# Optimization experiments

Hardware: AMD Instinct MI355X
Metric: run time of the kernel (lower is better)

## Reference

```python
import jax, jax.numpy as jnp
import numpy as np
import math


def _mirror_even(x):
    # even-symmetric extension: [..., H, W] -> [..., 2H, 2W]
    x = jnp.concatenate([x, jnp.flip(x, -1)], axis=-1)
    return jnp.concatenate([x, jnp.flip(x, -2)], axis=-2)


def _grad_img(x):
    # Fourier-domain spectral gradient on the even-symmetric extension,
    # matching PoissonCompositionLayer.grad_img (wx = arange(1,2W+1)-(W+1) = arange(-W,W)).
    H, W = x.shape[-2], x.shape[-1]
    kx = jnp.arange(-W, W)[None, :]          # [1, 2W]
    ky = jnp.arange(-H, H)[:, None]          # [2H, 1]
    dft = jnp.fft.fftshift(jnp.fft.fft2(_mirror_even(x)), axes=(-1, -2))
    gx = jnp.fft.ifft2(jnp.fft.fftshift((2j * math.pi / (2 * W)) * kx * dft, axes=(-1, -2))).real
    gy = jnp.fft.ifft2(jnp.fft.fftshift((2j * math.pi / (2 * H)) * ky * dft, axes=(-1, -2))).real
    return gx[..., :H, :W], gy[..., :H, :W]


def setup_inputs() -> dict:
    key = jax.random.key(0)
    k1, k2, k3 = jax.random.split(key, 3)
    B, C, H, W = 2, 3, 512, 512
    target = jax.random.normal(k1, (B, C, H, W), dtype=jnp.float32)
    source = jax.random.normal(k2, (B, C, H, W), dtype=jnp.float32)
    mask = jax.random.uniform(k3, (B, C, H, W), dtype=jnp.float32)
    return {"target": target, "source": source, "mask": mask}


def reference(target, source, mask):
    H, W = target.shape[-2], target.shape[-1]
    # composite gradient field
    gxt, gyt = _grad_img(target)
    gxs, gys = _grad_img(source)
    gx = (1.0 - mask) * gxt + mask * gxs
    gy = (1.0 - mask) * gyt + mask * gys
    # odd extension in x / even in y for gx; odd in y / even in x for gy
    gxp = jnp.concatenate([gx, -jnp.flip(gx, -1)], axis=-1)
    gxp = jnp.concatenate([gxp, jnp.flip(gxp, -2)], axis=-2)
    gyp = jnp.concatenate([gy, -jnp.flip(gy, -2)], axis=-2)
    gyp = jnp.concatenate([gyp, jnp.flip(gyp, -1)], axis=-1)
    dx = jnp.fft.fftshift(jnp.fft.fft2(gxp), axes=(-1, -2))
    dy = jnp.fft.fftshift(jnp.fft.fft2(gyp), axes=(-1, -2))
    # shifted frequency grids (DC sits at index [H, W])
    kx = jnp.arange(-W, W)[None, :]
    ky = jnp.arange(-H, H)[:, None]
    fx = 2j * math.pi * kx / (2 * W)
    fy = 2j * math.pi * ky / (2 * H)
    coeff = (fx * dx + fy * dy) / (fx ** 2 + fy ** 2 + 1e-10)
    coeff = coeff.at[..., H, W].set(0.0)  # zero DC component
    u = jnp.fft.ifft2(jnp.fft.fftshift(coeff, axes=(-1, -2)))
    res = u.real[..., :H, :W]
    # mean-matching on the unmasked region; original uses batch index 0's means for all batches
    inv = 1.0 - mask
    denom = jnp.sum(inv, axis=(-1, -2))                       # [B, C]
    mean1 = jnp.sum(target * inv, axis=(-1, -2)) / denom      # [B, C]
    mean2 = jnp.sum(res * inv, axis=(-1, -2)) / denom         # [B, C]
    return res + (mean1[0] - mean2[0])[None, :, None, None]
```

## Files before the change

kernel.cpp:

```cpp
#include <hip/hip_runtime.h>


#define CH 262144
#define NCH 6
#define NTOT (NCH*CH)

typedef _Float16 f16x8 __attribute__((ext_vector_type(8)));
typedef float f32x4  __attribute__((ext_vector_type(4)));

static constexpr float kPi        = 3.14159265358979323846f;
static constexpr float kPiOver512 = 0.006135923151542565f;
static constexpr float kPi2Norm   = 3.7649933338155804e-05f;
static constexpr float kInvHW     = 3.814697265625e-06f;

__device__ __forceinline__ void hst(float v, short* p) {
    *reinterpret_cast<_Float16*>(p) = (_Float16)v;
}

__device__ __forceinline__ float hfun(int k) {
    if (k == 0) return 0.f;
    float sgn = 1.f;
    if (k < 0) { k = -k; sgn = -1.f; }
    if (k > 512) { k = 1024 - k; sgn = -sgn; }
    float sv, cv;
    sincosf((float)k * (kPi / 1024.0f), &sv, &cv);
    float v = cv / sv;
    if (k & 1) v = -v;
    return sgn * v;
}

__global__ void build_tables(short* Mc, short* Ms, short* McT, short* GT) {
    int idx = blockIdx.x * blockDim.x + threadIdx.x;
    if (idx >= CH) return;
    int a = idx >> 9, b = idx & 511;
    int p1 = (a * (2 * b + 1)) & 2047;
    float s1, c1; sincosf((float)p1 * (kPi / 1024.0f), &s1, &c1);
    hst(c1, Mc + idx);
    hst(s1, Ms + idx);
    int p2 = (b * (2 * a + 1)) & 2047;
    float s2, c2; sincosf((float)p2 * (kPi / 1024.0f), &s2, &c2);
    hst(c2, McT + idx);
    float g = (kPi / 1024.0f) * (hfun(a + b + 1) + hfun(a - b));
    hst(g, GT + idx);
}

__device__ __forceinline__ void gl_lds16(const short* g, const short* l) {
    __builtin_amdgcn_global_load_lds(
        (const __attribute__((address_space(1))) void*)g,
        (__attribute__((address_space(3))) void*)l, 16, 0, 0);
}

#define FOFF(r, j) (((r) << 6) + 8 * ((j) ^ ((r) & 7)))

#define MFMA16(a, b, c) __builtin_amdgcn_mfma_f32_16x16x32_f16(a, b, c, 0, 0, 0)

template<int OM>
__global__ __launch_bounds__(256) void gemm_tn(
    const short* __restrict__ A0, int sA0, const short* __restrict__ B0, int sB0,
    float* __restrict__ Cf0, short* __restrict__ O0, int sC0,
    const short* __restrict__ A1, int sA1, const short* __restrict__ B1, int sB1,
    float* __restrict__ Cf1, short* __restrict__ O1, int sC1,
    int zsplit, const float* __restrict__ msk, float* __restrict__ redp)
{
    __shared__ short LS[2][2][4096];
    int z = blockIdx.z;
    const short *A, *B; float* Cf; short* O;
    if (z < zsplit) {
        A = A0 + (size_t)z * sA0; B = B0 + (size_t)z * sB0;
        Cf = Cf0 ? Cf0 + (size_t)z * sC0 : nullptr;
        O  = O0 ? O0 + (size_t)z * sC0 : nullptr;
    } else {
        int zz = z - zsplit;
        A = A1 + (size_t)zz * sA1; B = B1 + (size_t)zz * sB1;
        Cf = Cf1 ? Cf1 + (size_t)zz * sC1 : nullptr;
        O  = O1 ? O1 + (size_t)zz * sC1 : nullptr;
    }
    int tid = threadIdx.x;
    int l = tid & 63, w = tid >> 6;
    int m0 = blockIdx.y * 64, n0 = blockIdx.x * 64;

    int srow = w * 8 + (l >> 3);
    int skc  = (l & 7) ^ ((l >> 3) & 7);
    const short* gA = A + (size_t)(m0 + srow) * 512 + 8 * skc;
    const short* gB = B + (size_t)(n0 + srow) * 512 + 8 * skc;

    int wr = w >> 1, wc = w & 1;
    int lr = l & 15, lc = l >> 4;
    int rA0 = wr * 32 + lr, rA1 = rA0 + 16;
    int rB0 = wc * 32 + lr, rB1 = rB0 + 16;

    f32x4 a00 = {0,0,0,0}, a01 = a00, a10 = a00, a11 = a00;

#define STAGE_AB(nb, k0) \
    gl_lds16(gA + (k0), &LS[nb][0][w * 512]); \
    gl_lds16(gA + (k0) + 32 * 512, &LS[nb][0][w * 512 + 2048]); \
    gl_lds16(gB + (k0), &LS[nb][1][w * 512]); \
    gl_lds16(gB + (k0) + 32 * 512, &LS[nb][1][w * 512 + 2048]);

    STAGE_AB(0, 0)
    __syncthreads();

    for (int step = 0; step < 8; ++step) {
        int buf = step & 1;
        if (step < 7) { STAGE_AB(buf ^ 1, (step + 1) * 64) }
#pragma unroll
        for (int ks = 0; ks < 2; ++ks) {
            int j = lc + 4 * ks;
            f16x8 va0 = *(const f16x8*)&LS[buf][0][FOFF(rA0, j)];
            f16x8 va1 = *(const f16x8*)&LS[buf][0][FOFF(rA1, j)];
            f16x8 vb0 = *(const f16x8*)&LS[buf][1][FOFF(rB0, j)];
            f16x8 vb1 = *(const f16x8*)&LS[buf][1][FOFF(rB1, j)];
            a00 = MFMA16(va0, vb0, a00);
            a01 = MFMA16(va0, vb1, a01);
            a10 = MFMA16(va1, vb0, a10);
            a11 = MFMA16(va1, vb1, a11);
        }
        __syncthreads();
    }
#undef STAGE_AB

    int crow = m0 + wr * 32 + lc * 4;
    int ccol = n0 + wc * 32 + lr;
    const f32x4* accs[2][2] = {{&a00, &a01}, {&a10, &a11}};
    float lsum = 0.f;
#pragma unroll
    for (int q = 0; q < 2; ++q)
#pragma unroll
        for (int pp = 0; pp < 2; ++pp)
#pragma unroll
            for (int rr = 0; rr < 4; ++rr) {
                int idx = (crow + q * 16 + rr) * 512 + ccol + pp * 16;
                float v = (*accs[q][pp])[rr];
                if (OM == 1) {
                    hst(v, O + idx);
                } else {
                    Cf[idx] = v;
                    lsum += v * (1.0f - msk[(size_t)z * CH + idx]);
                }
            }
    if (OM == 2) {
        float* red = (float*)LS;
        red[tid] = lsum;
        __syncthreads();
        for (int s2 = 128; s2 > 0; s2 >>= 1) {
            if (tid < s2) red[tid] += red[tid + s2];
            __syncthreads();
        }
        if (tid == 0) redp[z * 64 + blockIdx.y * 8 + blockIdx.x] = red[0];
    }
}

__global__ __launch_bounds__(256) void gemm_l1(
    const short* __restrict__ dn, const short* __restrict__ dt,
    const short* __restrict__ GT, const float* __restrict__ msk,
    short* __restrict__ C_, short* __restrict__ D_)
{
    __shared__ short LS[2][2][4096];
    int z = blockIdx.z;
    bool gxp = z < 6;
    int zz = gxp ? z : z - 6;
    const short* A = (gxp ? dn : dt) + (size_t)zz * CH;
    const float* mz = msk + (size_t)zz * CH;

    int tid = threadIdx.x;
    int l = tid & 63, w = tid >> 6;
    int m0 = blockIdx.y * 64, n0 = blockIdx.x * 64;

    int srow = w * 8 + (l >> 3);
    int skc  = (l & 7) ^ ((l >> 3) & 7);
    const short* gA = A + (size_t)(m0 + srow) * 512 + 8 * skc;
    const short* gB = GT + (size_t)(n0 + srow) * 512 + 8 * skc;

    int wr = w >> 1, wc = w & 1;
    int lr = l & 15, lc = l >> 4;
    int rA0 = wr * 32 + lr, rA1 = rA0 + 16;
    int rB0 = wc * 32 + lr, rB1 = rB0 + 16;

    f32x4 a00 = {0,0,0,0}, a01 = a00, a10 = a00, a11 = a00;

#define STAGE_AB(nb, k0) \
    gl_lds16(gA + (k0), &LS[nb][0][w * 512]); \
    gl_lds16(gA + (k0) + 32 * 512, &LS[nb][0][w * 512 + 2048]); \
    gl_lds16(gB + (k0), &LS[nb][1][w * 512]); \
    gl_lds16(gB + (k0) + 32 * 512, &LS[nb][1][w * 512 + 2048]);

    STAGE_AB(0, 0)
    __syncthreads();

    for (int step = 0; step < 8; ++step) {
        int buf = step & 1;
        if (step < 7) { STAGE_AB(buf ^ 1, (step + 1) * 64) }
#pragma unroll
        for (int ks = 0; ks < 2; ++ks) {
            int j = lc + 4 * ks;
            f16x8 va0 = *(const f16x8*)&LS[buf][0][FOFF(rA0, j)];
            f16x8 va1 = *(const f16x8*)&LS[buf][0][FOFF(rA1, j)];
            f16x8 vb0 = *(const f16x8*)&LS[buf][1][FOFF(rB0, j)];
            f16x8 vb1 = *(const f16x8*)&LS[buf][1][FOFF(rB1, j)];
            a00 = MFMA16(va0, vb0, a00);
            a01 = MFMA16(va0, vb1, a01);
            a10 = MFMA16(va1, vb0, a10);
            a11 = MFMA16(va1, vb1, a11);
        }
        __syncthreads();
    }
#undef STAGE_AB

    const f32x4* accs[2][2] = {{&a00, &a01}, {&a10, &a11}};
    float* tile = (float*)LS;

    if (gxp) {
        short* o = C_ + (size_t)zz * CH;
#pragma unroll
        for (int q = 0; q < 2; ++q)
#pragma unroll
            for (int pp = 0; pp < 2; ++pp)
#pragma unroll
                for (int rr = 0; rr < 4; ++rr) {
                    int r = wr * 32 + lc * 4 + q * 16 + rr;
                    int c = wc * 32 + pp * 16 + lr;
                    float v = (*accs[q][pp])[rr] * mz[(size_t)(m0 + r) * 512 + n0 + c];
                    tile[c * 65 + r] = v;
                }
        __syncthreads();
#pragma unroll
        for (int pass = 0; pass < 16; ++pass) {
            int jj = pass * 4 + (tid >> 6);
            int ii = tid & 63;
            hst(tile[jj * 65 + ii], o + (n0 + jj) * 512 + m0 + ii);
        }
    } else {
        short* o = D_ + (size_t)zz * CH;
#pragma unroll
        for (int pass = 0; pass < 16; ++pass) {
            int ii = pass * 4 + (tid >> 6);
            int jj = tid & 63;
            tile[jj * 65 + ii] = mz[(size_t)(n0 + ii) * 512 + m0 + jj];
        }
        __syncthreads();
#pragma unroll
        for (int q = 0; q < 2; ++q)
#pragma unroll
            for (int pp = 0; pp < 2; ++pp)
#pragma unroll
                for (int rr = 0; rr < 4; ++rr) {
                    int r = wr * 32 + lc * 4 + q * 16 + rr;
                    int c = wc * 32 + pp * 16 + lr;
                    float v = (*accs[q][pp])[rr] * tile[r * 65 + c];
                    hst(v, o + (m0 + r) * 512 + n0 + c);
                }
    }
}

__global__ __launch_bounds__(256) void gemm_l3(
    const short* __restrict__ Ms, const short* __restrict__ Mc,
    const short* __restrict__ P, const short* __restrict__ Q,
    short* __restrict__ O_)
{
    __shared__ short LS[2][4][4096];
    int z = blockIdx.z;
    const short* pz = P + (size_t)z * CH;
    const short* qz = Q + (size_t)z * CH;
    short* o = O_ + (size_t)z * CH;

    int tid = threadIdx.x;
    int l = tid & 63, w = tid >> 6;
    int m0 = blockIdx.y * 64, n0 = blockIdx.x * 64;

    int srow = w * 8 + (l >> 3);
    int skc  = (l & 7) ^ ((l >> 3) & 7);
    size_t ga = (size_t)(m0 + srow) * 512 + 8 * skc;
    size_t gb = (size_t)(n0 + srow) * 512 + 8 * skc;
    const short* g0 = Ms + ga;
    const short* g1 = Mc + ga;
    const short* g2 = pz + gb;
    const short* g3 = qz + gb;

    int wr = w >> 1, wc = w & 1;
    int lr = l & 15, lc = l >> 4;
    int rA0 = wr * 32 + lr, rA1 = rA0 + 16;
    int rB0 = wc * 32 + lr, rB1 = rB0 + 16;

    f32x4 x00 = {0,0,0,0}, x01 = x00, x10 = x00, x11 = x00;
    f32x4 y00 = x00, y01 = x00, y10 = x00, y11 = x00;

#define STAGE_L3(nb, k0) \
    gl_lds16(g0 + (k0), &LS[nb][0][w * 512]); \
    gl_lds16(g0 + (k0) + 32 * 512, &LS[nb][0][w * 512 + 2048]); \
    gl_lds16(g1 + (k0), &LS[nb][1][w * 512]); \
    gl_lds16(g1 + (k0) + 32 * 512, &LS[nb][1][w * 512 + 2048]); \
    gl_lds16(g2 + (k0), &LS[nb][2][w * 512]); \
    gl_lds16(g2 + (k0) + 32 * 512, &LS[nb][2][w * 512 + 2048]); \
    gl_lds16(g3 + (k0), &LS[nb][3][w * 512]); \
    gl_lds16(g3 + (k0) + 32 * 512, &LS[nb][3][w * 512 + 2048]);

    STAGE_L3(0, 0)
    __syncthreads();

    for (int step = 0; step < 8; ++step) {
        int buf = step & 1;
        if (step < 7) { STAGE_L3(buf ^ 1, (step + 1) * 64) }
#pragma unroll
        for (int ks = 0; ks < 2; ++ks) {
            int j = lc + 4 * ks;
            f16x8 s0 = *(const f16x8*)&LS[buf][0][FOFF(rA0, j)];
            f16x8 s1 = *(const f16x8*)&LS[buf][0][FOFF(rA1, j)];
            f16x8 p0 = *(const f16x8*)&LS[buf][2][FOFF(rB0, j)];
            f16x8 p1 = *(const f16x8*)&LS[buf][2][FOFF(rB1, j)];
            x00 = MFMA16(s0, p0, x00);
            x01 = MFMA16(s0, p1, x01);
            x10 = MFMA16(s1, p0, x10);
            x11 = MFMA16(s1, p1, x11);
            f16x8 c0 = *(const f16x8*)&LS[buf][1][FOFF(rA0, j)];
            f16x8 c1 = *(const f16x8*)&LS[buf][1][FOFF(rA1, j)];
            f16x8 q0 = *(const f16x8*)&LS[buf][3][FOFF(rB0, j)];
            f16x8 q1 = *(const f16x8*)&LS[buf][3][FOFF(rB1, j)];
            y00 = MFMA16(c0, q0, y00);
            y01 = MFMA16(c0, q1, y01);
            y10 = MFMA16(c1, q0, y10);
            y11 = MFMA16(c1, q1, y11);
        }
        __syncthreads();
    }
#undef STAGE_L3

    int crow = m0 + wr * 32 + lc * 4;
    int ccol = n0 + wc * 32 + lr;
    const f32x4* xs[2][2] = {{&x00, &x01}, {&x10, &x11}};
    const f32x4* ys[2][2] = {{&y00, &y01}, {&y10, &y11}};
#pragma unroll
    for (int q = 0; q < 2; ++q)
#pragma unroll
        for (int pp = 0; pp < 2; ++pp) {
            int u = ccol + pp * 16;
            float eu = (u ? 2.0f : 1.0f) * kInvHW;
#pragma unroll
            for (int rr = 0; rr < 4; ++rr) {
                int v = crow + q * 16 + rr;
                float gx = (*xs[q][pp])[rr];
                float gy = (*ys[q][pp])[rr];
                float num = kPiOver512 * ((float)v * gx + (float)u * gy);
                float den = 1e-10f - kPi2Norm * (float)(u * u + v * v);
                float eps = (v ? 2.0f : 1.0f) * eu;
                hst(eps * num / den, o + v * 512 + u);
            }
        }
}

__global__ __launch_bounds__(256) void diff_split_red(
    const float* __restrict__ s, const float* __restrict__ t, const float* __restrict__ m,
    short* __restrict__ dn, short* __restrict__ dt,
    float* __restrict__ mt, float* __restrict__ mi)
{
    __shared__ float tile[32][33];
    __shared__ float red[512];
    int z = blockIdx.z;
    const float* sz = s + (size_t)z * CH;
    const float* tz = t + (size_t)z * CH;
    const float* mz = m + (size_t)z * CH;
    short* nh = dn + (size_t)z * CH;
    short* th = dt + (size_t)z * CH;
    int bx = blockIdx.x * 32, by = blockIdx.y * 32;
    int tx = threadIdx.x & 31, ty = threadIdx.x >> 5;
    float accT = 0.f, accI = 0.f;
    for (int r = ty; r < 32; r += 8) {
        int idx = (by + r) * 512 + bx + tx;
        float tv = tz[idx];
        float d = sz[idx] - tv;
        tile[r][tx] = d;
        hst(d, nh + idx);
        accT += tv;
        if (z < 3) accI += 1.0f - mz[idx];
    }
    __syncthreads();
    for (int r = ty; r < 32; r += 8) {
        hst(tile[tx][r], th + (bx + r) * 512 + by + tx);
    }
    int tid = threadIdx.x;
    red[tid] = accT; red[256 + tid] = accI;
    __syncthreads();
    for (int s2 = 128; s2 > 0; s2 >>= 1) {
        if (tid < s2) { red[tid] += red[tid + s2]; red[256 + tid] += red[256 + tid + s2]; }
        __syncthreads();
    }
    if (tid == 0) {
        int tileid = blockIdx.y * 16 + blockIdx.x;
        mt[z * 256 + tileid] = red[0];
        if (z < 3) mi[z * 256 + tileid] = red[256];
    }
}

__global__ __launch_bounds__(256) void final_out(
    const float* __restrict__ t, const float* __restrict__ U,
    const float* __restrict__ part, float* __restrict__ out)
{
    __shared__ float mtv[6], wmuv[3];
    int tid = threadIdx.x;
    if (tid < 6) {
        float s2 = 0.f;
        for (int k = 0; k < 256; ++k) s2 += part[tid * 256 + k];
        mtv[tid] = s2 * (1.0f / (float)CH);
    }
    if (tid >= 8 && tid < 11) {
        int c = tid - 8;
        float si = 0.f, su = 0.f;
        for (int k = 0; k < 256; ++k) si += part[1536 + c * 256 + k];
        for (int k = 0; k < 64; ++k) su += part[2304 + c * 64 + k];
        wmuv[c] = su / si;
    }
    __syncthreads();
    int n4 = NTOT / 4;
    for (int i = blockIdx.x * blockDim.x + tid; i < n4; i += gridDim.x * blockDim.x) {
        int z = i >> 16;
        int c = z % 3;
        float sh = -mtv[z] + mtv[c] - wmuv[c];
        float4 tv = ((const float4*)t)[i];
        float4 uv = ((const float4*)U)[i];
        ((float4*)out)[i] = make_float4(tv.x + uv.x + sh, tv.y + uv.y + sh,
                                        tv.z + uv.z + sh, tv.w + uv.w + sh);
    }
}

extern "C" void kernel_launch(void* const* d_in, const int* in_sizes, int n_in,
                              void* d_out, int out_size, void* d_ws, size_t ws_size,
                              hipStream_t stream) {
    const float* t = (const float*)d_in[0];
    const float* s = (const float*)d_in[1];
    const float* m = (const float*)d_in[2];
    float* out = (float*)d_out;
    float* F = (float*)d_ws;
    if (ws_size < (size_t)(21 * CH + 4096) * sizeof(float)) return;

    short* T = (short*)F;
    short *Mc = T, *Ms = T + (size_t)CH, *McT = T + 2 * (size_t)CH, *GT = T + 3 * (size_t)CH;
    short* A_ = (short*)(F + 2  * (size_t)CH);
    short* B_ = (short*)(F + 5  * (size_t)CH);
    short* C_ = (short*)(F + 8  * (size_t)CH);
    short* D_ = (short*)(F + 11 * (size_t)CH);
    float* F0  = F + 14 * (size_t)CH;
    float* part = F + 20 * (size_t)CH;

    build_tables<<<1024, 256, 0, stream>>>(Mc, Ms, McT, GT);

    diff_split_red<<<dim3(16, 16, 6), 256, 0, stream>>>(s, t, m, A_, B_,
                                                        part, part + 1536);

    gemm_l1<<<dim3(8, 8, 12), 256, 0, stream>>>(A_, B_, GT, m, C_, D_);

    gemm_tn<1><<<dim3(8, 8, 12), 256, 0, stream>>>(
        Mc, 0, C_, CH, nullptr, A_, CH,
        Ms, 0, D_, CH, nullptr, B_, CH, 6, nullptr, nullptr);

    gemm_l3<<<dim3(8, 8, 6), 256, 0, stream>>>(Ms, Mc, A_, B_, C_);

    gemm_tn<1><<<dim3(8, 8, 6), 256, 0, stream>>>(
        McT, 0, C_, CH, nullptr, D_, CH,
        McT, 0, C_, CH, nullptr, D_, CH, 6, nullptr, nullptr);

    gemm_tn<2><<<dim3(8, 8, 6), 256, 0, stream>>>(
        D_, CH, McT, 0, F0, nullptr, CH,
        D_, CH, McT, 0, F0, nullptr, CH, 6, m, part + 2304);

    final_out<<<768, 256, 0, stream>>>(t, F0, part, out);
}
```

Measured before the change: 70.39 us.

## Pre-swizzle constant DCT tables into MFMA fragment order and fuse table build

The constant cosine/sine/gradient tables are now generated directly in MFMA operand-fragment order, so every GEMM kernel reads them straight from global memory into registers instead of staging them through LDS. This halves the LDS staging traffic and LDS footprint per block. The separate table-building launch is merged into the difference/reduction kernel as an extra z-slice, removing one kernel launch. The cost is that the per-k-step direct global loads of table fragments now sit in the MFMA loop and may expose latency that LDS prefetch previously hid.

Measured after the change: 77.95 us. 10.7% more time.

```diff
diff --git a/kernel.cpp b/kernel.cpp
--- a/kernel.cpp
+++ b/kernel.cpp
@@ -29,21 +29,6 @@
     return sgn * v;
 }
 
-__global__ void build_tables(short* Mc, short* Ms, short* McT, short* GT) {
-    int idx = blockIdx.x * blockDim.x + threadIdx.x;
-    if (idx >= CH) return;
-    int a = idx >> 9, b = idx & 511;
-    int p1 = (a * (2 * b + 1)) & 2047;
-    float s1, c1; sincosf((float)p1 * (kPi / 1024.0f), &s1, &c1);
-    hst(c1, Mc + idx);
-    hst(s1, Ms + idx);
-    int p2 = (b * (2 * a + 1)) & 2047;
-    float s2, c2; sincosf((float)p2 * (kPi / 1024.0f), &s2, &c2);
-    hst(c2, McT + idx);
-    float g = (kPi / 1024.0f) * (hfun(a + b + 1) + hfun(a - b));
-    hst(g, GT + idx);
-}
-
 __device__ __forceinline__ void gl_lds16(const short* g, const short* l) {
     __builtin_amdgcn_global_load_lds(
         (const __attribute__((address_space(1))) void*)g,
@@ -51,27 +36,26 @@
 }
 
 #define FOFF(r, j) (((r) << 6) + 8 * ((j) ^ ((r) & 7)))
-
 #define MFMA16(a, b, c) __builtin_amdgcn_mfma_f32_16x16x32_f16(a, b, c, 0, 0, 0)
 
-template<int OM>
+template<int OM, int TA>
 __global__ __launch_bounds__(256) void gemm_tn(
-    const short* __restrict__ A0, int sA0, const short* __restrict__ B0, int sB0,
+    const short* __restrict__ T0, const short* __restrict__ X0, int sX0,
     float* __restrict__ Cf0, short* __restrict__ O0, int sC0,
-    const short* __restrict__ A1, int sA1, const short* __restrict__ B1, int sB1,
+    const short* __restrict__ T1, const short* __restrict__ X1, int sX1,
     float* __restrict__ Cf1, short* __restrict__ O1, int sC1,
     int zsplit, const float* __restrict__ msk, float* __restrict__ redp)
 {
-    __shared__ short LS[2][2][4096];
+    __shared__ short LS[2][4352];
     int z = blockIdx.z;
-    const short *A, *B; float* Cf; short* O;
+    const short *T, *X; float* Cf; short* O;
     if (z < zsplit) {
-        A = A0 + (size_t)z * sA0; B = B0 + (size_t)z * sB0;
+        T = T0; X = X0 + (size_t)z * sX0;
         Cf = Cf0 ? Cf0 + (size_t)z * sC0 : nullptr;
         O  = O0 ? O0 + (size_t)z * sC0 : nullptr;
     } else {
         int zz = z - zsplit;
-        A = A1 + (size_t)zz * sA1; B = B1 + (size_t)zz * sB1;
+        T = T1; X = X1 + (size_t)zz * sX1;
         Cf = Cf1 ? Cf1 + (size_t)zz * sC1 : nullptr;
         O  = O1 ? O1 + (size_t)zz * sC1 : nullptr;
     }
@@ -79,45 +63,53 @@
     int l = tid & 63, w = tid >> 6;
     int m0 = blockIdx.y * 64, n0 = blockIdx.x * 64;
 
+    int xbase = TA ? n0 : m0;
     int srow = w * 8 + (l >> 3);
     int skc  = (l & 7) ^ ((l >> 3) & 7);
-    const short* gA = A + (size_t)(m0 + srow) * 512 + 8 * skc;
-    const short* gB = B + (size_t)(n0 + srow) * 512 + 8 * skc;
+    const short* gX = X + (size_t)(xbase + srow) * 512 + 8 * skc;
 
     int wr = w >> 1, wc = w & 1;
     int lr = l & 15, lc = l >> 4;
-    int rA0 = wr * 32 + lr, rA1 = rA0 + 16;
-    int rB0 = wc * 32 + lr, rB1 = rB0 + 16;
+    int rX0 = (TA ? wc : wr) * 32 + lr, rX1 = rX0 + 16;
+    int ttb = (TA ? (m0 + wr * 32) : (n0 + wc * 32)) >> 4;
+    const short* Tw0 = T + (size_t)ttb * 8192 + l * 8;
+    const short* Tw1 = Tw0 + 8192;
 
     f32x4 a00 = {0,0,0,0}, a01 = a00, a10 = a00, a11 = a00;
 
-#define STAGE_AB(nb, k0) \
-    gl_lds16(gA + (k0), &LS[nb][0][w * 512]); \
-    gl_lds16(gA + (k0) + 32 * 512, &LS[nb][0][w * 512 + 2048]); \
-    gl_lds16(gB + (k0), &LS[nb][1][w * 512]); \
-    gl_lds16(gB + (k0) + 32 * 512, &LS[nb][1][w * 512 + 2048]);
-
-    STAGE_AB(0, 0)
+#define STAGE_X(nb, k0) \
+    gl_lds16(gX + (k0), &LS[nb][w * 512]); \
+    gl_lds16(gX + (k0) + 32 * 512, &LS[nb][w * 512 + 2048]);
+
+    STAGE_X(0, 0)
     __syncthreads();
 
     for (int step = 0; step < 8; ++step) {
         int buf = step & 1;
-        if (step < 7) { STAGE_AB(buf ^ 1, (step + 1) * 64) }
+        if (step < 7) { STAGE_X(buf ^ 1, (step + 1) * 64) }
 #pragma unroll
         for (int ks = 0; ks < 2; ++ks) {
             int j = lc + 4 * ks;
-            f16x8 va0 = *(const f16x8*)&LS[buf][0][FOFF(rA0, j)];
-            f16x8 va1 = *(const f16x8*)&LS[buf][0][FOFF(rA1, j)];
-            f16x8 vb0 = *(const f16x8*)&LS[buf][1][FOFF(rB0, j)];
-            f16x8 vb1 = *(const f16x8*)&LS[buf][1][FOFF(rB1, j)];
-            a00 = MFMA16(va0, vb0, a00);
-            a01 = MFMA16(va0, vb1, a01);
-            a10 = MFMA16(va1, vb0, a10);
-            a11 = MFMA16(va1, vb1, a11);
-        }
-        __syncthreads();
-    }
-#undef STAGE_AB
+            int kc = step * 2 + ks;
+            f16x8 xf0 = *(const f16x8*)&LS[buf][FOFF(rX0, j)];
+            f16x8 xf1 = *(const f16x8*)&LS[buf][FOFF(rX1, j)];
+            f16x8 tf0 = *(const f16x8*)(Tw0 + kc * 512);
+            f16x8 tf1 = *(const f16x8*)(Tw1 + kc * 512);
+            if constexpr (TA) {
+                a00 = MFMA16(tf0, xf0, a00);
+                a01 = MFMA16(tf0, xf1, a01);
+                a10 = MFMA16(tf1, xf0, a10);
+                a11 = MFMA16(tf1, xf1, a11);
+            } else {
+                a00 = MFMA16(xf0, tf0, a00);
+                a01 = MFMA16(xf0, tf1, a01);
+                a10 = MFMA16(xf1, tf0, a10);
+                a11 = MFMA16(xf1, tf1, a11);
+            }
+        }
+        __syncthreads();
+    }
+#undef STAGE_X
 
     int crow = m0 + wr * 32 + lc * 4;
     int ccol = n0 + wc * 32 + lr;
@@ -155,11 +147,11 @@
     const short* __restrict__ GT, const float* __restrict__ msk,
     short* __restrict__ C_, short* __restrict__ D_)
 {
-    __shared__ short LS[2][2][4096];
+    __shared__ short LS[2][4352];
     int z = blockIdx.z;
     bool gxp = z < 6;
     int zz = gxp ? z : z - 6;
-    const short* A = (gxp ? dn : dt) + (size_t)zz * CH;
+    const short* X = (gxp ? dn : dt) + (size_t)zz * CH;
     const float* mz = msk + (size_t)zz * CH;
 
     int tid = threadIdx.x;
@@ -168,43 +160,43 @@
 
     int srow = w * 8 + (l >> 3);
     int skc  = (l & 7) ^ ((l >> 3) & 7);
-    const short* gA = A + (size_t)(m0 + srow) * 512 + 8 * skc;
-    const short* gB = GT + (size_t)(n0 + srow) * 512 + 8 * skc;
+    const short* gX = X + (size_t)(m0 + srow) * 512 + 8 * skc;
 
     int wr = w >> 1, wc = w & 1;
     int lr = l & 15, lc = l >> 4;
-    int rA0 = wr * 32 + lr, rA1 = rA0 + 16;
-    int rB0 = wc * 32 + lr, rB1 = rB0 + 16;
+    int rX0 = wr * 32 + lr, rX1 = rX0 + 16;
+    int ttb = (n0 + wc * 32) >> 4;
+    const short* Tw0 = GT + (size_t)ttb * 8192 + l * 8;
+    const short* Tw1 = Tw0 + 8192;
 
     f32x4 a00 = {0,0,0,0}, a01 = a00, a10 = a00, a11 = a00;
 
-#define STAGE_AB(nb, k0) \
-    gl_lds16(gA + (k0), &LS[nb][0][w * 512]); \
-    gl_lds16(gA + (k0) + 32 * 512, &LS[nb][0][w * 512 + 2048]); \
-    gl_lds16(gB + (k0), &LS[nb][1][w * 512]); \
-    gl_lds16(gB + (k0) + 32 * 512, &LS[nb][1][w * 512 + 2048]);
-
-    STAGE_AB(0, 0)
+#define STAGE_X(nb, k0) \
+    gl_lds16(gX + (k0), &LS[nb][w * 512]); \
+    gl_lds16(gX + (k0) + 32 * 512, &LS[nb][w * 512 + 2048]);
+
+    STAGE_X(0, 0)
     __syncthreads();
 
     for (int step = 0; step < 8; ++step) {
         int buf = step & 1;
-        if (step < 7) { STAGE_AB(buf ^ 1, (step + 1) * 64) }
+        if (step < 7) { STAGE_X(buf ^ 1, (step + 1) * 64) }
 #pragma unroll
         for (int ks = 0; ks < 2; ++ks) {
             int j = lc + 4 * ks;
-            f16x8 va0 = *(const f16x8*)&LS[buf][0][FOFF(rA0, j)];
-            f16x8 va1 = *(const f16x8*)&LS[buf][0][FOFF(rA1, j)];
-            f16x8 vb0 = *(const f16x8*)&LS[buf][1][FOFF(rB0, j)];
-            f16x8 vb1 = *(const f16x8*)&LS[buf][1][FOFF(rB1, j)];
-            a00 = MFMA16(va0, vb0, a00);
-            a01 = MFMA16(va0, vb1, a01);
-            a10 = MFMA16(va1, vb0, a10);
-            a11 = MFMA16(va1, vb1, a11);
-        }
-        __syncthreads();
-    }
-#undef STAGE_AB
+            int kc = step * 2 + ks;
+            f16x8 xf0 = *(const f16x8*)&LS[buf][FOFF(rX0, j)];
+            f16x8 xf1 = *(const f16x8*)&LS[buf][FOFF(rX1, j)];
+            f16x8 tf0 = *(const f16x8*)(Tw0 + kc * 512);
+            f16x8 tf1 = *(const f16x8*)(Tw1 + kc * 512);
+            a00 = MFMA16(xf0, tf0, a00);
+            a01 = MFMA16(xf0, tf1, a01);
+            a10 = MFMA16(xf1, tf0, a10);
+            a11 = MFMA16(xf1, tf1, a11);
+        }
+        __syncthreads();
+    }
+#undef STAGE_X
 
     const f32x4* accs[2][2] = {{&a00, &a01}, {&a10, &a11}};
     float* tile = (float*)LS;
@@ -257,7 +249,7 @@
     const short* __restrict__ P, const short* __restrict__ Q,
     short* __restrict__ O_)
 {
-    __shared__ short LS[2][4][4096];
+    __shared__ short LS[2][2][4096];
     int z = blockIdx.z;
     const short* pz = P + (size_t)z * CH;
     const short* qz = Q + (size_t)z * CH;
@@ -269,52 +261,49 @@
 
     int srow = w * 8 + (l >> 3);
     int skc  = (l & 7) ^ ((l >> 3) & 7);
-    size_t ga = (size_t)(m0 + srow) * 512 + 8 * skc;
-    size_t gb = (size_t)(n0 + srow) * 512 + 8 * skc;
-    const short* g0 = Ms + ga;
-    const short* g1 = Mc + ga;
-    const short* g2 = pz + gb;
-    const short* g3 = qz + gb;
+    const short* gP = pz + (size_t)(n0 + srow) * 512 + 8 * skc;
+    const short* gQ = qz + (size_t)(n0 + srow) * 512 + 8 * skc;
 
     int wr = w >> 1, wc = w & 1;
     int lr = l & 15, lc = l >> 4;
-    int rA0 = wr * 32 + lr, rA1 = rA0 + 16;
     int rB0 = wc * 32 + lr, rB1 = rB0 + 16;
+    int ttb = (m0 + wr * 32) >> 4;
+    const short* ms0p = Ms + (size_t)ttb * 8192 + l * 8;
+    const short* ms1p = ms0p + 8192;
+    const short* mc0p = Mc + (size_t)ttb * 8192 + l * 8;
+    const short* mc1p = mc0p + 8192;
 
     f32x4 x00 = {0,0,0,0}, x01 = x00, x10 = x00, x11 = x00;
     f32x4 y00 = x00, y01 = x00, y10 = x00, y11 = x00;
 
-#define STAGE_L3(nb, k0) \
-    gl_lds16(g0 + (k0), &LS[nb][0][w * 512]); \
-    gl_lds16(g0 + (k0) + 32 * 512, &LS[nb][0][w * 512 + 2048]); \
-    gl_lds16(g1 + (k0), &LS[nb][1][w * 512]); \
-    gl_lds16(g1 + (k0) + 32 * 512, &LS[nb][1][w * 512 + 2048]); \
-    gl_lds16(g2 + (k0), &LS[nb][2][w * 512]); \
-    gl_lds16(g2 + (k0) + 32 * 512, &LS[nb][2][w * 512 + 2048]); \
-    gl_lds16(g3 + (k0), &LS[nb][3][w * 512]); \
-    gl_lds16(g3 + (k0) + 32 * 512, &LS[nb][3][w * 512 + 2048]);
-
-    STAGE_L3(0, 0)
+#define STAGE_PQ(nb, k0) \
+    gl_lds16(gP + (k0), &LS[nb][0][w * 512]); \
+    gl_lds16(gP + (k0) + 32 * 512, &LS[nb][0][w * 512 + 2048]); \
+    gl_lds16(gQ + (k0), &LS[nb][1][w * 512]); \
+    gl_lds16(gQ + (k0) + 32 * 512, &LS[nb][1][w * 512 + 2048]);
+
+    STAGE_PQ(0, 0)
     __syncthreads();
 
     for (int step = 0; step < 8; ++step) {
         int buf = step & 1;
-        if (step < 7) { STAGE_L3(buf ^ 1, (step + 1) * 64) }
+        if (step < 7) { STAGE_PQ(buf ^ 1, (step + 1) * 64) }
 #pragma unroll
         for (int ks = 0; ks < 2; ++ks) {
             int j = lc + 4 * ks;
-            f16x8 s0 = *(const f16x8*)&LS[buf][0][FOFF(rA0, j)];
-            f16x8 s1 = *(const f16x8*)&LS[buf][0][FOFF(rA1, j)];
-            f16x8 p0 = *(const f16x8*)&LS[buf][2][FOFF(rB0, j)];
-            f16x8 p1 = *(const f16x8*)&LS[buf][2][FOFF(rB1, j)];
+            int kc = step * 2 + ks;
+            f16x8 p0 = *(const f16x8*)&LS[buf][0][FOFF(rB0, j)];
+            f16x8 p1 = *(const f16x8*)&LS[buf][0][FOFF(rB1, j)];
+            f16x8 s0 = *(const f16x8*)(ms0p + kc * 512);
+            f16x8 s1 = *(const f16x8*)(ms1p + kc * 512);
             x00 = MFMA16(s0, p0, x00);
             x01 = MFMA16(s0, p1, x01);
             x10 = MFMA16(s1, p0, x10);
             x11 = MFMA16(s1, p1, x11);
-            f16x8 c0 = *(const f16x8*)&LS[buf][1][FOFF(rA0, j)];
-            f16x8 c1 = *(const f16x8*)&LS[buf][1][FOFF(rA1, j)];
-            f16x8 q0 = *(const f16x8*)&LS[buf][3][FOFF(rB0, j)];
-            f16x8 q1 = *(const f16x8*)&LS[buf][3][FOFF(rB1, j)];
+            f16x8 q0 = *(const f16x8*)&LS[buf][1][FOFF(rB0, j)];
+            f16x8 q1 = *(const f16x8*)&LS[buf][1][FOFF(rB1, j)];
+            f16x8 c0 = *(const f16x8*)(mc0p + kc * 512);
+            f16x8 c1 = *(const f16x8*)(mc1p + kc * 512);
             y00 = MFMA16(c0, q0, y00);
             y01 = MFMA16(c0, q1, y01);
             y10 = MFMA16(c1, q0, y10);
@@ -322,7 +311,7 @@
         }
         __syncthreads();
     }
-#undef STAGE_L3
+#undef STAGE_PQ
 
     int crow = m0 + wr * 32 + lc * 4;
     int ccol = n0 + wc * 32 + lr;
@@ -347,14 +336,44 @@
         }
 }
 
-__global__ __launch_bounds__(256) void diff_split_red(
+__global__ __launch_bounds__(256) void diff_split_tab(
     const float* __restrict__ s, const float* __restrict__ t, const float* __restrict__ m,
     short* __restrict__ dn, short* __restrict__ dt,
+    short* __restrict__ Mc, short* __restrict__ Ms,
+    short* __restrict__ McT, short* __restrict__ GT,
     float* __restrict__ mt, float* __restrict__ mi)
 {
+    int z = blockIdx.z;
+    if (z == 6) {
+        int bid = blockIdx.y * 16 + blockIdx.x;
+        if (bid >= 128) return;
+        int g = bid * 256 + threadIdx.x;
+        int f = g >> 6, lane = g & 63;
+        int r  = ((f >> 4) << 4) | (lane & 15);
+        int kb = ((f & 15) << 5) | ((lane >> 4) << 3);
+        f16x8 vmc, vms, vmct, vgt;
+#pragma unroll
+        for (int e = 0; e < 8; ++e) {
+            int k = kb + e;
+            int p1 = (r * (2 * k + 1)) & 2047;
+            float s1, c1; sincosf((float)p1 * (kPi / 1024.0f), &s1, &c1);
+            int p2 = (k * (2 * r + 1)) & 2047;
+            float s2, c2; sincosf((float)p2 * (kPi / 1024.0f), &s2, &c2);
+            float gt = (kPi / 1024.0f) * (hfun(r + k + 1) + hfun(r - k));
+            vmc[e]  = (_Float16)c1;
+            vms[e]  = (_Float16)s1;
+            vmct[e] = (_Float16)c2;
+            vgt[e]  = (_Float16)gt;
+        }
+        *(f16x8*)(Mc  + (size_t)g * 8) = vmc;
+        *(f16x8*)(Ms  + (size_t)g * 8) = vms;
+        *(f16x8*)(McT + (size_t)g * 8) = vmct;
+        *(f16x8*)(GT  + (size_t)g * 8) = vgt;
+        return;
+    }
+
     __shared__ float tile[32][33];
     __shared__ float red[512];
-    int z = blockIdx.z;
     const float* sz = s + (size_t)z * CH;
     const float* tz = t + (size_t)z * CH;
     const float* mz = m + (size_t)z * CH;
@@ -440,26 +459,25 @@
     float* F0  = F + 14 * (size_t)CH;
     float* part = F + 20 * (size_t)CH;
 
-    build_tables<<<1024, 256, 0, stream>>>(Mc, Ms, McT, GT);
-
-    diff_split_red<<<dim3(16, 16, 6), 256, 0, stream>>>(s, t, m, A_, B_,
+    diff_split_tab<<<dim3(16, 16, 7), 256, 0, stream>>>(s, t, m, A_, B_,
+                                                        Mc, Ms, McT, GT,
                                                         part, part + 1536);
 
     gemm_l1<<<dim3(8, 8, 12), 256, 0, stream>>>(A_, B_, GT, m, C_, D_);
 
-    gemm_tn<1><<<dim3(8, 8, 12), 256, 0, stream>>>(
-        Mc, 0, C_, CH, nullptr, A_, CH,
-        Ms, 0, D_, CH, nullptr, B_, CH, 6, nullptr, nullptr);
+    gemm_tn<1, 1><<<dim3(8, 8, 12), 256, 0, stream>>>(
+        Mc, C_, CH, nullptr, A_, CH,
+        Ms, D_, CH, nullptr, B_, CH, 6, nullptr, nullptr);
 
     gemm_l3<<<dim3(8, 8, 6), 256, 0, stream>>>(Ms, Mc, A_, B_, C_);
 
-    gemm_tn<1><<<dim3(8, 8, 6), 256, 0, stream>>>(
-        McT, 0, C_, CH, nullptr, D_, CH,
-        McT, 0, C_, CH, nullptr, D_, CH, 6, nullptr, nullptr);
-
-    gemm_tn<2><<<dim3(8, 8, 6), 256, 0, stream>>>(
-        D_, CH, McT, 0, F0, nullptr, CH,
-        D_, CH, McT, 0, F0, nullptr, CH, 6, m, part + 2304);
+    gemm_tn<1, 1><<<dim3(8, 8, 6), 256, 0, stream>>>(
+        McT, C_, CH, nullptr, D_, CH,
+        McT, C_, CH, nullptr, D_, CH, 6, nullptr, nullptr);
+
+    gemm_tn<2, 0><<<dim3(8, 8, 6), 256, 0, stream>>>(
+        McT, D_, CH, F0, nullptr, CH,
+        McT, D_, CH, F0, nullptr, CH, 6, m, part + 2304);
 
     final_out<<<768, 256, 0, stream>>>(t, F0, part, out);
 }
```

## Fuse table build into split kernel and remap GEMM blocks across XCDs

Applied to the files above, without the earlier changes.

The separate build_tables launch is folded into the diff/split kernel as an extra z-slice, where each of 256 blocks computes four table entries per thread. This removes one kernel launch and lets table generation run alongside the split work. All GEMM kernels also remap their linear block id so that consecutive blocks stay on the same XCD, aiming for better L2 locality of shared operand tiles. The remap spreads work differently across chiplets and adds integer divides per block. The table slice uses fewer threads, each doing four entries serially.

Result: faster. 64.40 us (median of 2 runs) (-8.5%).

```diff
diff --git a/kernel.cpp b/kernel.cpp
--- a/kernel.cpp
+++ b/kernel.cpp
@@ -29,19 +29,14 @@
     return sgn * v;
 }
 
-__global__ void build_tables(short* Mc, short* Ms, short* McT, short* GT) {
-    int idx = blockIdx.x * blockDim.x + threadIdx.x;
-    if (idx >= CH) return;
-    int a = idx >> 9, b = idx & 511;
-    int p1 = (a * (2 * b + 1)) & 2047;
-    float s1, c1; sincosf((float)p1 * (kPi / 1024.0f), &s1, &c1);
-    hst(c1, Mc + idx);
-    hst(s1, Ms + idx);
-    int p2 = (b * (2 * a + 1)) & 2047;
-    float s2, c2; sincosf((float)p2 * (kPi / 1024.0f), &s2, &c2);
-    hst(c2, McT + idx);
-    float g = (kPi / 1024.0f) * (hfun(a + b + 1) + hfun(a - b));
-    hst(g, GT + idx);
+__device__ __forceinline__ void xcd_remap(int& bx, int& by, int& bz) {
+    int nx = gridDim.x, ny = gridDim.y;
+    int nwg = nx * ny * gridDim.z;
+    int w = blockIdx.x + nx * (blockIdx.y + ny * blockIdx.z);
+    int s = (w & 7) * (nwg >> 3) + (w >> 3);
+    bx = s % nx; s /= nx;
+    by = s % ny;
+    bz = s / ny;
 }
 
 __device__ __forceinline__ void gl_lds16(const short* g, const short* l) {
@@ -51,7 +46,6 @@
 }
 
 #define FOFF(r, j) (((r) << 6) + 8 * ((j) ^ ((r) & 7)))
-
 #define MFMA16(a, b, c) __builtin_amdgcn_mfma_f32_16x16x32_f16(a, b, c, 0, 0, 0)
 
 template<int OM>
@@ -63,7 +57,8 @@
     int zsplit, const float* __restrict__ msk, float* __restrict__ redp)
 {
     __shared__ short LS[2][2][4096];
-    int z = blockIdx.z;
+    int bx, by, z;
+    xcd_remap(bx, by, z);
     const short *A, *B; float* Cf; short* O;
     if (z < zsplit) {
         A = A0 + (size_t)z * sA0; B = B0 + (size_t)z * sB0;
@@ -77,7 +72,7 @@
     }
     int tid = threadIdx.x;
     int l = tid & 63, w = tid >> 6;
-    int m0 = blockIdx.y * 64, n0 = blockIdx.x * 64;
+    int m0 = by * 64, n0 = bx * 64;
 
     int srow = w * 8 + (l >> 3);
     int skc  = (l & 7) ^ ((l >> 3) & 7);
@@ -146,7 +141,7 @@
             if (tid < s2) red[tid] += red[tid + s2];
             __syncthreads();
         }
-        if (tid == 0) redp[z * 64 + blockIdx.y * 8 + blockIdx.x] = red[0];
+        if (tid == 0) redp[z * 64 + by * 8 + bx] = red[0];
     }
 }
 
@@ -156,7 +151,8 @@
     short* __restrict__ C_, short* __restrict__ D_)
 {
     __shared__ short LS[2][2][4096];
-    int z = blockIdx.z;
+    int bx, by, z;
+    xcd_remap(bx, by, z);
     bool gxp = z < 6;
     int zz = gxp ? z : z - 6;
     const short* A = (gxp ? dn : dt) + (size_t)zz * CH;
@@ -164,7 +160,7 @@
 
     int tid = threadIdx.x;
     int l = tid & 63, w = tid >> 6;
-    int m0 = blockIdx.y * 64, n0 = blockIdx.x * 64;
+    int m0 = by * 64, n0 = bx * 64;
 
     int srow = w * 8 + (l >> 3);
     int skc  = (l & 7) ^ ((l >> 3) & 7);
@@ -258,14 +254,15 @@
     short* __restrict__ O_)
 {
     __shared__ short LS[2][4][4096];
-    int z = blockIdx.z;
+    int bx, by, z;
+    xcd_remap(bx, by, z);
     const short* pz = P + (size_t)z * CH;
     const short* qz = Q + (size_t)z * CH;
     short* o = O_ + (size_t)z * CH;
 
     int tid = threadIdx.x;
     int l = tid & 63, w = tid >> 6;
-    int m0 = blockIdx.y * 64, n0 = blockIdx.x * 64;
+    int m0 = by * 64, n0 = bx * 64;
 
     int srow = w * 8 + (l >> 3);
     int skc  = (l & 7) ^ ((l >> 3) & 7);
@@ -347,14 +344,36 @@
         }
 }
 
-__global__ __launch_bounds__(256) void diff_split_red(
+__global__ __launch_bounds__(256) void diff_split_tab(
     const float* __restrict__ s, const float* __restrict__ t, const float* __restrict__ m,
     short* __restrict__ dn, short* __restrict__ dt,
+    short* __restrict__ Mc, short* __restrict__ Ms,
+    short* __restrict__ McT, short* __restrict__ GT,
     float* __restrict__ mt, float* __restrict__ mi)
 {
+    int z = blockIdx.z;
+    if (z == 6) {
+        int bid = blockIdx.y * 16 + blockIdx.x;
+        int base = (bid * 256 + threadIdx.x) * 4;
+#pragma unroll
+        for (int e = 0; e < 4; ++e) {
+            int idx = base + e;
+            int a = idx >> 9, b = idx & 511;
+            int p1 = (a * (2 * b + 1)) & 2047;
+            float s1, c1; sincosf((float)p1 * (kPi / 1024.0f), &s1, &c1);
+            hst(c1, Mc + idx);
+            hst(s1, Ms + idx);
+            int p2 = (b * (2 * a + 1)) & 2047;
+            float s2, c2; sincosf((float)p2 * (kPi / 1024.0f), &s2, &c2);
+            hst(c2, McT + idx);
+            float g = (kPi / 1024.0f) * (hfun(a + b + 1) + hfun(a - b));
+            hst(g, GT + idx);
+        }
+        return;
+    }
+
     __shared__ float tile[32][33];
     __shared__ float red[512];
-    int z = blockIdx.z;
     const float* sz = s + (size_t)z * CH;
     const float* tz = t + (size_t)z * CH;
     const float* mz = m + (size_t)z * CH;
@@ -440,9 +459,8 @@
     float* F0  = F + 14 * (size_t)CH;
     float* part = F + 20 * (size_t)CH;
 
-    build_tables<<<1024, 256, 0, stream>>>(Mc, Ms, McT, GT);
-
-    diff_split_red<<<dim3(16, 16, 6), 256, 0, stream>>>(s, t, m, A_, B_,
+    diff_split_tab<<<dim3(16, 16, 7), 256, 0, stream>>>(s, t, m, A_, B_,
+                                                        Mc, Ms, McT, GT,
                                                         part, part + 1536);
 
     gemm_l1<<<dim3(8, 8, 12), 256, 0, stream>>>(A_, B_, GT, m, C_, D_);
```
